# Kernel tuning notes

Measured on AMD Instinct MI355X. Metric: run time of the kernel, lower is better.

Reference implementation:

```python
import jax, jax.numpy as jnp
import numpy as np
from jax import lax


def _conv2d(x, w, b, pad):
    out = lax.conv_general_dilated(x, w, window_strides=(1, 1),
                                   padding=[(pad, pad), (pad, pad)])
    return out + b[None, :, None, None]


def _modulated_deform_conv(x, off_w, off_b, w, b, k, pad):
    """Modulated deformable conv (deformable_groups=1, stride=1, 'same' pad)."""
    B, C, H, W = x.shape
    K2 = k * k
    # offset/mask conv: 3*K2 channels -> (dy, dx, mask_logits)
    om = _conv2d(x, off_w, off_b, pad)              # [B, 3*K2, H, W]
    dy, dx, mlog = om[:, :K2], om[:, K2:2 * K2], om[:, 2 * K2:]
    mask = jax.nn.sigmoid(mlog)                     # [B, K2, H, W]

    xp = jnp.pad(x, ((0, 0), (0, 0), (pad, pad), (pad, pad)))
    Hp, Wp = H + 2 * pad, W + 2 * pad
    Ho, Wo = H, W                                   # stride 1, pad = k//2

    ky, kx = jnp.meshgrid(jnp.arange(k), jnp.arange(k), indexing='ij')
    ky = ky.reshape(1, K2, 1, 1).astype(x.dtype)
    kx = kx.reshape(1, K2, 1, 1).astype(x.dtype)
    iy = jnp.arange(Ho, dtype=x.dtype).reshape(1, 1, Ho, 1)
    ix = jnp.arange(Wo, dtype=x.dtype).reshape(1, 1, 1, Wo)

    py = iy + ky + dy                               # [B, K2, Ho, Wo] sample y (padded coords)
    px = ix + kx + dx                               # [B, K2, Ho, Wo] sample x

    y0f = jnp.floor(py); x0f = jnp.floor(px)
    ty = py - y0f; tx = px - x0f
    y0 = y0f.astype(jnp.int32); x0 = x0f.astype(jnp.int32)
    y1 = y0 + 1; x1 = x0 + 1

    xp_flat = xp.reshape(B, C, Hp * Wp)

    def gather(yi, xi):
        valid = ((yi >= 0) & (yi < Hp) & (xi >= 0) & (xi < Wp)).astype(x.dtype)
        yc = jnp.clip(yi, 0, Hp - 1)
        xc = jnp.clip(xi, 0, Wp - 1)
        idx = (yc * Wp + xc).reshape(B, 1, K2 * Ho * Wo)
        v = jnp.take_along_axis(xp_flat, idx, axis=2).reshape(B, C, K2, Ho, Wo)
        return v * valid[:, None]                   # zero-pad outside

    w00 = ((1 - ty) * (1 - tx))[:, None]
    w01 = ((1 - ty) * tx)[:, None]
    w10 = (ty * (1 - tx))[:, None]
    w11 = (ty * tx)[:, None]

    cols = (gather(y0, x0) * w00 + gather(y0, x1) * w01 +
            gather(y1, x0) * w10 + gather(y1, x1) * w11)
    cols = cols * mask[:, None]                     # [B, C, K2, Ho, Wo]

    O = w.shape[0]
    out = jnp.einsum('bckhw,ock->bohw', cols, w.reshape(O, C, K2))
    return out + b[None, :, None, None]


def setup_inputs() -> dict:
    key = jax.random.key(0)
    ks = jax.random.split(key, 12)
    B, Cin, H, W = 8, 64, 56, 56
    Ch = 128  # out_channels // 2

    def rn(k, shape, scale):
        return jax.random.normal(k, shape, dtype=jnp.float32) * scale

    return {
        'x': rn(ks[0], (B, Cin, H, W), 1.0),
        'w3': rn(ks[1], (Ch, Cin, 3, 3), 0.05),
        'b3': rn(ks[2], (Ch,), 0.05),
        'off3_w': rn(ks[3], (3 * 9, Cin, 3, 3), 0.01),
        'off3_b': rn(ks[4], (3 * 9,), 0.01),
        'w5': rn(ks[5], (Ch, Cin, 5, 5), 0.03),
        'b5': rn(ks[6], (Ch,), 0.05),
        'off5_w': rn(ks[7], (3 * 25, Cin, 5, 5), 0.01),
        'off5_b': rn(ks[8], (3 * 25,), 0.01),
        'sub_w': rn(ks[9], (Ch, Cin, 1, 1), 0.1),
        'sub_b': rn(ks[10], (Ch,), 0.05),
    }


def reference(x, w3, b3, off3_w, off3_b, w5, b5, off5_w, off5_b, sub_w, sub_b):
    x3 = _modulated_deform_conv(x, off3_w, off3_b, w3, b3, k=3, pad=1)
    x5 = _modulated_deform_conv(x, off5_w, off5_b, w5, b5, k=5, pad=2)
    xs = _conv2d(x, sub_w, sub_b, pad=0)            # 1x1 shortcut projection
    x3 = x3 + xs
    x5 = x5 + xs
    out = jnp.concatenate((x3, x5), axis=1)
    return jax.nn.relu(out)
```

## Files before the change

### kernel.cpp

```cpp
#include <hip/hip_runtime.h>
#include <hip/hip_bf16.h>
#include <math.h>

typedef __attribute__((ext_vector_type(8))) short short8;
typedef __attribute__((ext_vector_type(4))) float f32x4;

#define US_XP    0
#define N_XP     (8*60*60*64)
#define US_WOFF  (US_XP + N_XP)
#define N_WOFF   (26*2*8*64*8)
#define US_W5    (US_WOFF + N_WOFF)
#define N_W5     (26*2*8*64*8)
#define US_W3    (US_W5 + N_W5)
#define N_W3     (10*2*8*64*8)
#define US_TOT   (US_W3 + N_W3)
#define FB_BYTES (((US_TOT*2) + 15) & ~15)
#define F_BOM    0
#define F_B5     128
#define F_B3     256
#define N_ITEMS  (8*34*3136)
#define F_OFFS   384
#define F_WTS    (F_OFFS + N_ITEMS*4)

__device__ __forceinline__ unsigned short f2bf(float f) {
    union { float f; unsigned u; } v; v.f = f;
    unsigned r = v.u + 0x7FFFu + ((v.u >> 16) & 1u);
    return (unsigned short)(r >> 16);
}
__device__ __forceinline__ unsigned pack2(float lo, float hi) {
    __hip_bfloat162 h = __float22bfloat162_rn(make_float2(lo, hi));
    return *(unsigned*)&h;
}
__device__ __forceinline__ unsigned blend2(unsigned a, unsigned b, unsigned c, unsigned d,
                                           float w00, float w01, float w10, float w11) {
    float lo = __uint_as_float(a << 16) * w00 + __uint_as_float(b << 16) * w01
             + __uint_as_float(c << 16) * w10 + __uint_as_float(d << 16) * w11;
    float hi = __uint_as_float(a & 0xffff0000u) * w00 + __uint_as_float(b & 0xffff0000u) * w01
             + __uint_as_float(c & 0xffff0000u) * w10 + __uint_as_float(d & 0xffff0000u) * w11;
    return pack2(lo, hi);
}

__global__ __launch_bounds__(256) void prep_kernel(
    const float* __restrict__ x,
    const float* __restrict__ w3, const float* __restrict__ b3,
    const float* __restrict__ off3w, const float* __restrict__ off3b,
    const float* __restrict__ w5, const float* __restrict__ b5,
    const float* __restrict__ off5w, const float* __restrict__ off5b,
    const float* __restrict__ subw, const float* __restrict__ subb,
    unsigned short* __restrict__ us, float* __restrict__ fb)
{
    const int NTOT = US_TOT + 384;
    for (int i = blockIdx.x*256 + threadIdx.x; i < NTOT; i += gridDim.x*256) {
        if (i < US_TOT) {
            float v = 0.f;
            if (i < US_WOFF) {
                int c = i & 63, t = i >> 6;
                int xx = t % 60; t /= 60;
                int yy = t % 60; int b = t / 60;
                int y = yy - 2, xc = xx - 2;
                if ((unsigned)y < 56u && (unsigned)xc < 56u)
                    v = x[((b*64 + c)*56 + y)*56 + xc];
            } else {
                int j, mode;
                if (i < US_W5)      { j = i - US_WOFF; mode = 0; }
                else if (i < US_W3) { j = i - US_W5;   mode = 1; }
                else                { j = i - US_W3;   mode = 2; }
                int j8   = j & 7;
                int lane = (j >> 3) & 63;
                int oct  = (j >> 9) & 7;
                int kt   = (j >> 12) & 1;
                int tap  = j >> 13;
                int oc   = oct*16 + (lane & 15);
                int c    = kt*32 + (lane >> 4)*8 + j8;
                if (mode == 0) {
                    if (oc < 27 && tap < 25) {
                        int ky = tap/5, kx = tap%5;
                        if (ky>=1 && ky<=3 && kx>=1 && kx<=3)
                            v = off3w[((oc*64 + c)*3 + (ky-1))*3 + (kx-1)];
                    } else if (oc >= 27 && oc < 102 && tap < 25) {
                        v = off5w[((oc-27)*64 + c)*25 + tap];
                    }
                } else if (mode == 1) {
                    v = (tap < 25) ? w5[(oc*64 + c)*25 + tap] : subw[oc*64 + c];
                } else {
                    v = (tap < 9) ? w3[(oc*64 + c)*9 + tap] : subw[oc*64 + c];
                }
            }
            us[i] = f2bf(v);
        } else {
            int fj = i - US_TOT;
            float v;
            if (fj < 128)      v = (fj < 27) ? off3b[fj] : ((fj < 102) ? off5b[fj-27] : 0.f);
            else if (fj < 256) { int o = fj-128; v = b5[o] + subb[o]; }
            else               { int o = fj-256; v = b3[o] + subb[o]; }
            fb[fj] = v;
        }
    }
}

__global__ __launch_bounds__(256, 6) void convo3(
    const unsigned short* __restrict__ xp,
    const unsigned short* __restrict__ wp, const float* __restrict__ bias,
    int4* __restrict__ offs, uint2* __restrict__ wts)
{
    const int b    = blockIdx.y;
    const int pix0 = blockIdx.x * 32;
    const int lane = threadIdx.x & 63;
    const int wave = threadIdx.x >> 6;
    const int r15 = lane & 15, q4 = lane >> 4;
    const int cg  = lane & 7,  pr = lane >> 3;

    __shared__ __align__(16) unsigned short cols[2][2][32*72];

    f32x4 acc[2][2] = {{{0.f,0.f,0.f,0.f},{0.f,0.f,0.f,0.f}},
                       {{0.f,0.f,0.f,0.f},{0.f,0.f,0.f,0.f}}};

    const char* xb = (const char*)(xp + (size_t)b*(60*60*64));
    const int px  = wave*8 + pr;
    const int pix = pix0 + px;
    const int oy  = pix/56, ox = pix - oy*56;
    const int coff = (((oy+2)*60) + ox + 2) << 7;

    uint4 G0, G1;
    auto issue = [&](int ta, int tb) {
        int ka = 0, kb = 0;
        if (ta < 25) { int ky = ta/5, kx = ta - ky*5; ka = ((ky-2)*60 + (kx-2)) << 7; }
        if (tb < 25) { int ky = tb/5, kx = tb - ky*5; kb = ((ky-2)*60 + (kx-2)) << 7; }
        G0 = *(const uint4*)(xb + coff + ka + cg*16);
        G1 = *(const uint4*)(xb + coff + kb + cg*16);
    };
    auto commit = [&](unsigned short* bufa, unsigned short* bufb) {
        *(uint4*)&bufa[px*72 + cg*8] = G0;
        *(uint4*)&bufb[px*72 + cg*8] = G1;
    };
    auto gemm = [&](int tap, const unsigned short* buf) {
#pragma unroll
        for (int kt = 0; kt < 2; ++kt) {
            short8 A0 = *(const short8*)(wp + ((size_t)((tap*2+kt)*8 + wave*2    )*64 + lane)*8);
            short8 A1 = *(const short8*)(wp + ((size_t)((tap*2+kt)*8 + wave*2 + 1)*64 + lane)*8);
#pragma unroll
            for (int pt = 0; pt < 2; ++pt) {
                short8 Bf = *(const short8*)(buf + (pt*16 + r15)*72 + kt*32 + q4*8);
                acc[0][pt] = __builtin_amdgcn_mfma_f32_16x16x32_bf16(A0, Bf, acc[0][pt], 0, 0, 0);
                acc[1][pt] = __builtin_amdgcn_mfma_f32_16x16x32_bf16(A1, Bf, acc[1][pt], 0, 0, 0);
            }
        }
    };

    issue(0, 1);
    commit(cols[0][0], cols[0][1]);
    __syncthreads();
    for (int r = 0; r < 13; ++r) {
        if (r + 1 < 13) issue(2*r+2, 2*r+3);
        gemm(2*r,   cols[r&1][0]);
        gemm(2*r+1, cols[r&1][1]);
        if (r + 1 < 13) commit(cols[(r+1)&1][0], cols[(r+1)&1][1]);
        __syncthreads();
    }

    float* omt = (float*)cols;
#pragma unroll
    for (int i = 0; i < 2; ++i)
#pragma unroll
    for (int pt = 0; pt < 2; ++pt)
#pragma unroll
    for (int reg = 0; reg < 4; ++reg) {
        const int oc = (wave*2 + i)*16 + q4*4 + reg;
        const int p2 = pt*16 + r15;
        omt[oc*32 + p2] = acc[i][pt][reg] + bias[oc];
    }
    __syncthreads();

    const int tid = threadIdx.x;
#pragma unroll
    for (int itr = 0; itr < 5; ++itr) {
        const int idx = itr*256 + tid;
        if (idx >= 34*32) break;
        const int t  = idx >> 5;
        const int p2 = idx & 31;
        const int pix2 = pix0 + p2;
        const int oy2 = pix2/56, ox2 = pix2 - oy2*56;
        int ky, kx, cdy, cdx, cml, HP, SH;
        if (t < 25) { ky = t/5; kx = t%5; cdy = 27+t; cdx = 52+t; cml = 77+t; HP = 60; SH = 0; }
        else { int tt = t-25; ky = tt/3; kx = tt%3; cdy = tt; cdx = 9+tt; cml = 18+tt; HP = 58; SH = 1; }
        const float dy = omt[cdy*32 + p2];
        const float dx = omt[cdx*32 + p2];
        const float ml = omt[cml*32 + p2];
        const float mask = 1.f / (1.f + __expf(-ml));
        const float py = (float)(oy2 + ky) + dy;
        const float qx = (float)(ox2 + kx) + dx;
        const float y0f = floorf(py), x0f = floorf(qx);
        const float ty = py - y0f, tx = qx - x0f;
        const int y0 = (int)y0f, x0 = (int)x0f, y1 = y0+1, x1 = x0+1;
        float w00 = (1.f-ty)*(1.f-tx)*mask;
        float w01 = (1.f-ty)*tx*mask;
        float w10 = ty*(1.f-tx)*mask;
        float w11 = ty*tx*mask;
        const bool vy0 = (unsigned)y0 < (unsigned)HP, vy1 = (unsigned)y1 < (unsigned)HP;
        const bool vx0 = (unsigned)x0 < (unsigned)HP, vx1 = (unsigned)x1 < (unsigned)HP;
        if (!(vy0 && vx0)) w00 = 0.f;
        if (!(vy0 && vx1)) w01 = 0.f;
        if (!(vy1 && vx0)) w10 = 0.f;
        if (!(vy1 && vx1)) w11 = 0.f;
        const int yc0 = min(max(y0,0),HP-1)+SH, yc1 = min(max(y1,0),HP-1)+SH;
        const int xc0 = min(max(x0,0),HP-1)+SH, xc1 = min(max(x1,0),HP-1)+SH;
        const int mi = (b*34 + t)*3136 + pix2;
        offs[mi] = make_int4((yc0*60+xc0)<<7, (yc0*60+xc1)<<7, (yc1*60+xc0)<<7, (yc1*60+xc1)<<7);
        wts[mi]  = make_uint2(pack2(w00,w01), pack2(w10,w11));
    }
}

__global__ __launch_bounds__(256, 5) void convd3(
    const unsigned short* __restrict__ xp,
    const int4* __restrict__ offs, const uint2* __restrict__ wts,
    float* __restrict__ out,
    const unsigned short* __restrict__ wp5, const float* __restrict__ bias5,
    const unsigned short* __restrict__ wp3, const float* __restrict__ bias3)
{
    const int kind  = blockIdx.z;
    const unsigned short* wp = kind ? wp3 : wp5;
    const float* bias = kind ? bias3 : bias5;
    const int R     = kind ? 5  : 13;
    const int K2    = kind ? 9  : 25;
    const int tofs  = kind ? 25 : 0;
    const int outc0 = kind ? 0  : 128;

    const int b    = blockIdx.y;
    const int pix0 = blockIdx.x * 32;
    const int lane = threadIdx.x & 63;
    const int wave = threadIdx.x >> 6;
    const int r15 = lane & 15, q4 = lane >> 4;
    const int cg  = lane & 7,  pr = lane >> 3;

    __shared__ __align__(16) unsigned short cols[2][2][32*72];

    f32x4 acc[2][2] = {{{0.f,0.f,0.f,0.f},{0.f,0.f,0.f,0.f}},
                       {{0.f,0.f,0.f,0.f},{0.f,0.f,0.f,0.f}}};

    const char* xb = (const char*)(xp + (size_t)b*(60*60*64));
    const int px  = wave*8 + pr;
    const int pix = pix0 + px;
    const int oy  = pix/56, ox = pix - oy*56;
    const int coff  = (((oy+2)*60) + ox + 2) << 7;
    const int mbase = (b*34 + tofs)*3136 + pix;

    uint4 C0[4], C1[4];
    uint2 WC0, WC1;
    int4  MO0, MO1;
    uint2 MW0, MW1;

    auto load_meta = [&](int ta, int tb) {
        const int a  = min(ta, K2-1) * 3136;
        const int bb = min(tb, K2-1) * 3136;
        MO0 = offs[mbase + a];  MW0 = wts[mbase + a];
        MO1 = offs[mbase + bb]; MW1 = wts[mbase + bb];
    };
    auto issue = [&](int ta, int tb) {
        if (ta >= K2) {
            C0[0] = *(const uint4*)(xb + coff + cg*16);
        } else {
            WC0 = MW0;
            C0[0] = *(const uint4*)(xb + MO0.x + cg*16);
            C0[1] = *(const uint4*)(xb + MO0.y + cg*16);
            C0[2] = *(const uint4*)(xb + MO0.z + cg*16);
            C0[3] = *(const uint4*)(xb + MO0.w + cg*16);
        }
        if (tb >= K2) {
            C1[0] = *(const uint4*)(xb + coff + cg*16);
        } else {
            WC1 = MW1;
            C1[0] = *(const uint4*)(xb + MO1.x + cg*16);
            C1[1] = *(const uint4*)(xb + MO1.y + cg*16);
            C1[2] = *(const uint4*)(xb + MO1.z + cg*16);
            C1[3] = *(const uint4*)(xb + MO1.w + cg*16);
        }
    };
    auto commit = [&](int ta, int tb, unsigned short* bufa, unsigned short* bufb) {
        uint4 res;
        if (ta >= K2) {
            res = C0[0];
        } else {
            const float w00 = __uint_as_float(WC0.x << 16);
            const float w01 = __uint_as_float(WC0.x & 0xffff0000u);
            const float w10 = __uint_as_float(WC0.y << 16);
            const float w11 = __uint_as_float(WC0.y & 0xffff0000u);
            res.x = blend2(C0[0].x, C0[1].x, C0[2].x, C0[3].x, w00, w01, w10, w11);
            res.y = blend2(C0[0].y, C0[1].y, C0[2].y, C0[3].y, w00, w01, w10, w11);
            res.z = blend2(C0[0].z, C0[1].z, C0[2].z, C0[3].z, w00, w01, w10, w11);
            res.w = blend2(C0[0].w, C0[1].w, C0[2].w, C0[3].w, w00, w01, w10, w11);
        }
        *(uint4*)&bufa[px*72 + cg*8] = res;
        if (tb >= K2) {
            res = C1[0];
        } else {
            const float w00 = __uint_as_float(WC1.x << 16);
            const float w01 = __uint_as_float(WC1.x & 0xffff0000u);
            const float w10 = __uint_as_float(WC1.y << 16);
            const float w11 = __uint_as_float(WC1.y & 0xffff0000u);
            res.x = blend2(C1[0].x, C1[1].x, C1[2].x, C1[3].x, w00, w01, w10, w11);
            res.y = blend2(C1[0].y, C1[1].y, C1[2].y, C1[3].y, w00, w01, w10, w11);
            res.z = blend2(C1[0].z, C1[1].z, C1[2].z, C1[3].z, w00, w01, w10, w11);
            res.w = blend2(C1[0].w, C1[1].w, C1[2].w, C1[3].w, w00, w01, w10, w11);
        }
        *(uint4*)&bufb[px*72 + cg*8] = res;
    };
    auto gemm = [&](int tap, const unsigned short* buf) {
#pragma unroll
        for (int kt = 0; kt < 2; ++kt) {
            short8 A0 = *(const short8*)(wp + ((size_t)((tap*2+kt)*8 + wave*2    )*64 + lane)*8);
            short8 A1 = *(const short8*)(wp + ((size_t)((tap*2+kt)*8 + wave*2 + 1)*64 + lane)*8);
#pragma unroll
            for (int pt = 0; pt < 2; ++pt) {
                short8 Bf = *(const short8*)(buf + (pt*16 + r15)*72 + kt*32 + q4*8);
                acc[0][pt] = __builtin_amdgcn_mfma_f32_16x16x32_bf16(A0, Bf, acc[0][pt], 0, 0, 0);
                acc[1][pt] = __builtin_amdgcn_mfma_f32_16x16x32_bf16(A1, Bf, acc[1][pt], 0, 0, 0);
            }
        }
    };

    load_meta(0, 1);
    issue(0, 1);
    load_meta(2, 3);
    commit(0, 1, cols[0][0], cols[0][1]);
    __syncthreads();

    for (int r = 0; r < R; ++r) {
        if (r + 1 < R) {
            issue(2*r+2, 2*r+3);
            load_meta(2*r+4, 2*r+5);
        }
        gemm(2*r,   cols[r&1][0]);
        gemm(2*r+1, cols[r&1][1]);
        if (r + 1 < R)
            commit(2*r+2, 2*r+3, cols[(r+1)&1][0], cols[(r+1)&1][1]);
        __syncthreads();
    }

#pragma unroll
    for (int i = 0; i < 2; ++i)
#pragma unroll
    for (int pt = 0; pt < 2; ++pt)
#pragma unroll
    for (int reg = 0; reg < 4; ++reg) {
        const int oc  = (wave*2 + i)*16 + q4*4 + reg;
        const int p2  = pix0 + pt*16 + r15;
        float v = fmaxf(acc[i][pt][reg] + bias[oc], 0.f);
        out[((size_t)b*256 + outc0 + oc)*3136 + p2] = v;
    }
}

extern "C" void kernel_launch(void* const* d_in, const int* in_sizes, int n_in,
                              void* d_out, int out_size, void* d_ws, size_t ws_size,
                              hipStream_t stream)
{
    (void)in_sizes; (void)n_in; (void)out_size; (void)ws_size;
    const float* x     = (const float*)d_in[0];
    const float* w3    = (const float*)d_in[1];
    const float* b3    = (const float*)d_in[2];
    const float* off3w = (const float*)d_in[3];
    const float* off3b = (const float*)d_in[4];
    const float* w5    = (const float*)d_in[5];
    const float* b5    = (const float*)d_in[6];
    const float* off5w = (const float*)d_in[7];
    const float* off5b = (const float*)d_in[8];
    const float* subw  = (const float*)d_in[9];
    const float* subb  = (const float*)d_in[10];

    unsigned short* us = (unsigned short*)d_ws;
    float* fb   = (float*)((char*)d_ws + FB_BYTES);
    int4*  offs = (int4*)(fb + F_OFFS);
    uint2* wts  = (uint2*)(fb + F_WTS);
    float* out  = (float*)d_out;

    prep_kernel<<<dim3(1024), dim3(256), 0, stream>>>(
        x, w3, b3, off3w, off3b, w5, b5, off5w, off5b, subw, subb, us, fb);

    convo3<<<dim3(98, 8), dim3(256), 0, stream>>>(
        us + US_XP, us + US_WOFF, fb + F_BOM, offs, wts);

    convd3<<<dim3(98, 8, 2), dim3(256), 0, stream>>>(
        us + US_XP, offs, wts, out,
        us + US_W5, fb + F_B5, us + US_W3, fb + F_B3);
}
```

Before: 159.7 us.

## Split input prep into smem transpose, prefetch weight fragments in deform GEMM

The combined prep kernel is split in two. A new transpose kernel stages NCHW fp32 input tiles in shared memory and writes NHWC bf16 with 16-byte stores, after a memset that zeroes the padded buffer. A separate kernel now handles only the weight packing. In the deformable GEMM kernel, the MFMA A-fragments for the next round are preloaded into registers alongside the gather commit, offset metadata is double-buffered, and launch bounds drop from 5 to 3 blocks per CU. The extra register use lowers occupancy, and the added memset and launch bring their own overhead.

```diff
diff --git a/kernel.cpp b/kernel.cpp
--- a/kernel.cpp
+++ b/kernel.cpp
@@ -40,8 +40,33 @@
     return pack2(lo, hi);
 }
 
-__global__ __launch_bounds__(256) void prep_kernel(
-    const float* __restrict__ x,
+__global__ __launch_bounds__(256) void xpose(const float* __restrict__ x,
+                                             unsigned short* __restrict__ xp)
+{
+    __shared__ float ld[64*65];
+    const int b   = blockIdx.y;
+    const int px0 = blockIdx.x * 64;
+    const int t   = threadIdx.x;
+#pragma unroll
+    for (int c0 = 0; c0 < 64; c0 += 4) {
+        const int c = c0 + (t >> 6);
+        const int p = t & 63;
+        ld[c*65 + p] = x[((size_t)(b*64 + c))*3136 + px0 + p];
+    }
+    __syncthreads();
+    const int lp = t >> 2;
+    const int ch0 = (t & 3) * 16;
+    const int px = px0 + lp;
+    const int oy = px/56, ox = px - oy*56;
+    unsigned short* dst = xp + ((size_t)b*3600 + (oy+2)*60 + (ox+2))*64 + ch0;
+    unsigned short tmp[16];
+#pragma unroll
+    for (int k = 0; k < 16; ++k) tmp[k] = f2bf(ld[(ch0 + k)*65 + lp]);
+    *(uint4*)dst       = *(uint4*)&tmp[0];
+    *(uint4*)(dst + 8) = *(uint4*)&tmp[8];
+}
+
+__global__ __launch_bounds__(256) void prep_w(
     const float* __restrict__ w3, const float* __restrict__ b3,
     const float* __restrict__ off3w, const float* __restrict__ off3b,
     const float* __restrict__ w5, const float* __restrict__ b5,
@@ -50,41 +75,32 @@
     unsigned short* __restrict__ us, float* __restrict__ fb)
 {
     const int NTOT = US_TOT + 384;
-    for (int i = blockIdx.x*256 + threadIdx.x; i < NTOT; i += gridDim.x*256) {
+    for (int i = US_WOFF + blockIdx.x*256 + threadIdx.x; i < NTOT; i += gridDim.x*256) {
         if (i < US_TOT) {
             float v = 0.f;
-            if (i < US_WOFF) {
-                int c = i & 63, t = i >> 6;
-                int xx = t % 60; t /= 60;
-                int yy = t % 60; int b = t / 60;
-                int y = yy - 2, xc = xx - 2;
-                if ((unsigned)y < 56u && (unsigned)xc < 56u)
-                    v = x[((b*64 + c)*56 + y)*56 + xc];
+            int j, mode;
+            if (i < US_W5)      { j = i - US_WOFF; mode = 0; }
+            else if (i < US_W3) { j = i - US_W5;   mode = 1; }
+            else                { j = i - US_W3;   mode = 2; }
+            int j8   = j & 7;
+            int lane = (j >> 3) & 63;
+            int oct  = (j >> 9) & 7;
+            int kt   = (j >> 12) & 1;
+            int tap  = j >> 13;
+            int oc   = oct*16 + (lane & 15);
+            int c    = kt*32 + (lane >> 4)*8 + j8;
+            if (mode == 0) {
+                if (oc < 27 && tap < 25) {
+                    int ky = tap/5, kx = tap%5;
+                    if (ky>=1 && ky<=3 && kx>=1 && kx<=3)
+                        v = off3w[((oc*64 + c)*3 + (ky-1))*3 + (kx-1)];
+                } else if (oc >= 27 && oc < 102 && tap < 25) {
+                    v = off5w[((oc-27)*64 + c)*25 + tap];
+                }
+            } else if (mode == 1) {
+                v = (tap < 25) ? w5[(oc*64 + c)*25 + tap] : subw[oc*64 + c];
             } else {
-                int j, mode;
-                if (i < US_W5)      { j = i - US_WOFF; mode = 0; }
-                else if (i < US_W3) { j = i - US_W5;   mode = 1; }
-                else                { j = i - US_W3;   mode = 2; }
-                int j8   = j & 7;
-                int lane = (j >> 3) & 63;
-                int oct  = (j >> 9) & 7;
-                int kt   = (j >> 12) & 1;
-                int tap  = j >> 13;
-                int oc   = oct*16 + (lane & 15);
-                int c    = kt*32 + (lane >> 4)*8 + j8;
-                if (mode == 0) {
-                    if (oc < 27 && tap < 25) {
-                        int ky = tap/5, kx = tap%5;
-                        if (ky>=1 && ky<=3 && kx>=1 && kx<=3)
-                            v = off3w[((oc*64 + c)*3 + (ky-1))*3 + (kx-1)];
-                    } else if (oc >= 27 && oc < 102 && tap < 25) {
-                        v = off5w[((oc-27)*64 + c)*25 + tap];
-                    }
-                } else if (mode == 1) {
-                    v = (tap < 25) ? w5[(oc*64 + c)*25 + tap] : subw[oc*64 + c];
-                } else {
-                    v = (tap < 9) ? w3[(oc*64 + c)*9 + tap] : subw[oc*64 + c];
-                }
+                v = (tap < 9) ? w3[(oc*64 + c)*9 + tap] : subw[oc*64 + c];
             }
             us[i] = f2bf(v);
         } else {
@@ -210,14 +226,14 @@
     }
 }
 
-__global__ __launch_bounds__(256, 5) void convd3(
+__global__ __launch_bounds__(256, 3) void convd5(
     const unsigned short* __restrict__ xp,
     const int4* __restrict__ offs, const uint2* __restrict__ wts,
     float* __restrict__ out,
     const unsigned short* __restrict__ wp5, const float* __restrict__ bias5,
     const unsigned short* __restrict__ wp3, const float* __restrict__ bias3)
 {
-    const int kind  = blockIdx.z;
+    const int kind = blockIdx.z;
     const unsigned short* wp = kind ? wp3 : wp5;
     const float* bias = kind ? bias3 : bias5;
     const int R     = kind ? 5  : 13;
@@ -246,36 +262,37 @@
 
     uint4 C0[4], C1[4];
     uint2 WC0, WC1;
-    int4  MO0, MO1;
-    uint2 MW0, MW1;
-
-    auto load_meta = [&](int ta, int tb) {
+    int4  MOc0, MOc1, MOn0, MOn1;
+    uint2 MWc0, MWc1, MWn0, MWn1;
+    short8 Aa[8];
+
+    auto loadMetaN = [&](int ta, int tb) {
         const int a  = min(ta, K2-1) * 3136;
         const int bb = min(tb, K2-1) * 3136;
-        MO0 = offs[mbase + a];  MW0 = wts[mbase + a];
-        MO1 = offs[mbase + bb]; MW1 = wts[mbase + bb];
+        MOn0 = offs[mbase + a];  MWn0 = wts[mbase + a];
+        MOn1 = offs[mbase + bb]; MWn1 = wts[mbase + bb];
     };
     auto issue = [&](int ta, int tb) {
         if (ta >= K2) {
             C0[0] = *(const uint4*)(xb + coff + cg*16);
         } else {
-            WC0 = MW0;
-            C0[0] = *(const uint4*)(xb + MO0.x + cg*16);
-            C0[1] = *(const uint4*)(xb + MO0.y + cg*16);
-            C0[2] = *(const uint4*)(xb + MO0.z + cg*16);
-            C0[3] = *(const uint4*)(xb + MO0.w + cg*16);
+            WC0 = MWc0;
+            C0[0] = *(const uint4*)(xb + MOc0.x + cg*16);
+            C0[1] = *(const uint4*)(xb + MOc0.y + cg*16);
+            C0[2] = *(const uint4*)(xb + MOc0.z + cg*16);
+            C0[3] = *(const uint4*)(xb + MOc0.w + cg*16);
         }
         if (tb >= K2) {
             C1[0] = *(const uint4*)(xb + coff + cg*16);
         } else {
-            WC1 = MW1;
-            C1[0] = *(const uint4*)(xb + MO1.x + cg*16);
-            C1[1] = *(const uint4*)(xb + MO1.y + cg*16);
-            C1[2] = *(const uint4*)(xb + MO1.z + cg*16);
-            C1[3] = *(const uint4*)(xb + MO1.w + cg*16);
-        }
-    };
-    auto commit = [&](int ta, int tb, unsigned short* bufa, unsigned short* bufb) {
+            WC1 = MWc1;
+            C1[0] = *(const uint4*)(xb + MOc1.x + cg*16);
+            C1[1] = *(const uint4*)(xb + MOc1.y + cg*16);
+            C1[2] = *(const uint4*)(xb + MOc1.z + cg*16);
+            C1[3] = *(const uint4*)(xb + MOc1.w + cg*16);
+        }
+    };
+    auto commit = [&](int ta, int tb, unsigned short* ba, unsigned short* bb) {
         uint4 res;
         if (ta >= K2) {
             res = C0[0];
@@ -289,7 +306,7 @@
             res.z = blend2(C0[0].z, C0[1].z, C0[2].z, C0[3].z, w00, w01, w10, w11);
             res.w = blend2(C0[0].w, C0[1].w, C0[2].w, C0[3].w, w00, w01, w10, w11);
         }
-        *(uint4*)&bufa[px*72 + cg*8] = res;
+        *(uint4*)&ba[px*72 + cg*8] = res;
         if (tb >= K2) {
             res = C1[0];
         } else {
@@ -302,37 +319,49 @@
             res.z = blend2(C1[0].z, C1[1].z, C1[2].z, C1[3].z, w00, w01, w10, w11);
             res.w = blend2(C1[0].w, C1[1].w, C1[2].w, C1[3].w, w00, w01, w10, w11);
         }
-        *(uint4*)&bufb[px*72 + cg*8] = res;
-    };
-    auto gemm = [&](int tap, const unsigned short* buf) {
-#pragma unroll
-        for (int kt = 0; kt < 2; ++kt) {
-            short8 A0 = *(const short8*)(wp + ((size_t)((tap*2+kt)*8 + wave*2    )*64 + lane)*8);
-            short8 A1 = *(const short8*)(wp + ((size_t)((tap*2+kt)*8 + wave*2 + 1)*64 + lane)*8);
+        *(uint4*)&bb[px*72 + cg*8] = res;
+    };
+    auto loadA = [&](int r) {
+#pragma unroll
+        for (int tt = 0; tt < 2; ++tt)
+#pragma unroll
+        for (int kt = 0; kt < 2; ++kt)
+#pragma unroll
+        for (int i = 0; i < 2; ++i)
+            Aa[tt*4+kt*2+i] = *(const short8*)(wp + ((size_t)(((2*r+tt)*2+kt)*8 + wave*2 + i)*64 + lane)*8);
+    };
+    auto gemmT = [&](int tt, const unsigned short* buf) {
+#pragma unroll
+        for (int kt = 0; kt < 2; ++kt)
 #pragma unroll
             for (int pt = 0; pt < 2; ++pt) {
-                short8 Bf = *(const short8*)(buf + (pt*16 + r15)*72 + kt*32 + q4*8);
-                acc[0][pt] = __builtin_amdgcn_mfma_f32_16x16x32_bf16(A0, Bf, acc[0][pt], 0, 0, 0);
-                acc[1][pt] = __builtin_amdgcn_mfma_f32_16x16x32_bf16(A1, Bf, acc[1][pt], 0, 0, 0);
+                short8 B = *(const short8*)(buf + (pt*16 + r15)*72 + kt*32 + q4*8);
+                acc[0][pt] = __builtin_amdgcn_mfma_f32_16x16x32_bf16(Aa[tt*4+kt*2+0], B, acc[0][pt], 0, 0, 0);
+                acc[1][pt] = __builtin_amdgcn_mfma_f32_16x16x32_bf16(Aa[tt*4+kt*2+1], B, acc[1][pt], 0, 0, 0);
             }
-        }
-    };
-
-    load_meta(0, 1);
+    };
+
+    loadMetaN(0, 1);
+    MOc0 = MOn0; MWc0 = MWn0; MOc1 = MOn1; MWc1 = MWn1;
     issue(0, 1);
-    load_meta(2, 3);
+    loadMetaN(2, 3);
+    loadA(0);
     commit(0, 1, cols[0][0], cols[0][1]);
     __syncthreads();
 
     for (int r = 0; r < R; ++r) {
-        if (r + 1 < R) {
+        const bool more = (r + 1 < R);
+        if (more) {
+            MOc0 = MOn0; MWc0 = MWn0; MOc1 = MOn1; MWc1 = MWn1;
             issue(2*r+2, 2*r+3);
-            load_meta(2*r+4, 2*r+5);
-        }
-        gemm(2*r,   cols[r&1][0]);
-        gemm(2*r+1, cols[r&1][1]);
-        if (r + 1 < R)
+            loadMetaN(2*r+4, 2*r+5);
+        }
+        gemmT(0, cols[r&1][0]);
+        gemmT(1, cols[r&1][1]);
+        if (more) {
+            loadA(r + 1);
             commit(2*r+2, 2*r+3, cols[(r+1)&1][0], cols[(r+1)&1][1]);
+        }
         __syncthreads();
     }
 
@@ -342,8 +371,8 @@
     for (int pt = 0; pt < 2; ++pt)
 #pragma unroll
     for (int reg = 0; reg < 4; ++reg) {
-        const int oc  = (wave*2 + i)*16 + q4*4 + reg;
-        const int p2  = pix0 + pt*16 + r15;
+        const int oc = (wave*2 + i)*16 + q4*4 + reg;
+        const int p2 = pix0 + pt*16 + r15;
         float v = fmaxf(acc[i][pt][reg] + bias[oc], 0.f);
         out[((size_t)b*256 + outc0 + oc)*3136 + p2] = v;
     }
@@ -372,13 +401,15 @@
     uint2* wts  = (uint2*)(fb + F_WTS);
     float* out  = (float*)d_out;
 
-    prep_kernel<<<dim3(1024), dim3(256), 0, stream>>>(
-        x, w3, b3, off3w, off3b, w5, b5, off5w, off5b, subw, subb, us, fb);
+    hipMemsetAsync(us + US_XP, 0, (size_t)N_XP * 2, stream);
+    xpose<<<dim3(49, 8), dim3(256), 0, stream>>>(x, us + US_XP);
+    prep_w<<<dim3(512), dim3(256), 0, stream>>>(
+        w3, b3, off3w, off3b, w5, b5, off5w, off5b, subw, subb, us, fb);
 
     convo3<<<dim3(98, 8), dim3(256), 0, stream>>>(
         us + US_XP, us + US_WOFF, fb + F_BOM, offs, wts);
 
-    convd3<<<dim3(98, 8, 2), dim3(256), 0, stream>>>(
+    convd5<<<dim3(98, 8, 2), dim3(256), 0, stream>>>(
         us + US_XP, offs, wts, out,
         us + US_W5, fb + F_B5, us + US_W3, fb + F_B3);
 }
```

Measured after the change: 156.8 us. No clear change (-1.8%).
